# Kernel optimization log

Hardware: AMD Instinct MI355X
Metric: run time of the kernel (lower is better)

The kernel has to match this reference:

```python
import jax, jax.numpy as jnp
import numpy as np

LN_EPS = 1e-5
RMS_EPS = 1e-5

B, T, D = 4, 2048, 1024
H, DK, DV = 4, 256, 512            # head_k_dim = D/H, head_v_dim = expand_v * head_k_dim (expand_v=2)
KDIM, VDIM = H * DK, H * DV        # 1024, 2048
FFN = 4096                          # int(d_model * ffn_ratio)
CONV = 4


def _layernorm(x, w, b):
    mu = jnp.mean(x, -1, keepdims=True)
    var = jnp.mean(jnp.square(x - mu), -1, keepdims=True)
    return (x - mu) * jax.lax.rsqrt(var + LN_EPS) * w + b


def _short_conv_silu(x, w):
    # causal depthwise conv, kernel size K, then SiLU. x: [B,T,C], w: [C,K]
    K = w.shape[1]
    xp = jnp.pad(x, ((0, 0), (K - 1, 0), (0, 0)))
    y = sum(xp[:, i:i + x.shape[1], :] * w[:, i] for i in range(K))
    return jax.nn.silu(y)


def _l2norm(x):
    return x * jax.lax.rsqrt(jnp.sum(jnp.square(x), -1, keepdims=True) + 1e-6)


def _gated_delta_rule(q, k, v, g, beta):
    # q,k: [B,T,H,DK]; v: [B,T,H,DV]; g,beta: [B,T,H]
    # S_t = exp(g_t)*S_{t-1} + k_t (beta_t*(v_t - k_t^T exp(g_t) S_{t-1}))^T ; o_t = q_t^T S_t
    def step(S, inp):
        qt, kt, vt, gt, bt = inp
        S = S * jnp.exp(gt)[..., None, None]          # [B,H,DK,DV]
        mem = jnp.einsum('bhk,bhkv->bhv', kt, S)
        delta = (vt - mem) * bt[..., None]
        S = S + jnp.einsum('bhk,bhv->bhkv', kt, delta)
        o = jnp.einsum('bhk,bhkv->bhv', qt, S)
        return S, o
    S0 = jnp.zeros((q.shape[0], H, DK, DV), q.dtype)
    xs = (q.transpose(1, 0, 2, 3), k.transpose(1, 0, 2, 3), v.transpose(1, 0, 2, 3),
          g.transpose(1, 0, 2), beta.transpose(1, 0, 2))
    _, o = jax.lax.scan(step, S0, xs)
    return o.transpose(1, 0, 2, 3)  # [B,T,H,DV]


def setup_inputs() -> dict:
    key = jax.random.key(0)
    ks = jax.random.split(key, 24)
    n = lambda k, shp, s=0.02: jax.random.normal(k, shp, dtype=jnp.float32) * s
    return {
        'x': jax.random.normal(ks[0], (B, T, D), dtype=jnp.float32),
        'Wq': n(ks[1], (D, KDIM)), 'Wk': n(ks[2], (D, KDIM)), 'Wv': n(ks[3], (D, VDIM)),
        'Wa': n(ks[4], (D, H)), 'Wb': n(ks[5], (D, H)), 'Wg': n(ks[6], (D, VDIM)),
        'conv_q_w': n(ks[7], (KDIM, CONV), 0.2), 'conv_k_w': n(ks[8], (KDIM, CONV), 0.2),
        'conv_v_w': n(ks[9], (VDIM, CONV), 0.2),
        'A_log': jnp.log(jax.random.uniform(ks[10], (H,), minval=1.0, maxval=16.0, dtype=jnp.float32)),
        'dt_bias': jax.random.uniform(ks[11], (H,), minval=0.0, maxval=0.5, dtype=jnp.float32),
        'o_norm_w': jnp.ones((DV,), jnp.float32),
        'Wo': n(ks[12], (VDIM, D)),
        'ln1_w': jnp.ones((D,), jnp.float32), 'ln1_b': jnp.zeros((D,), jnp.float32),
        'ln2_w': jnp.ones((D,), jnp.float32), 'ln2_b': jnp.zeros((D,), jnp.float32),
        'ffn_w1': n(ks[13], (D, FFN)), 'ffn_b1': jnp.zeros((FFN,), jnp.float32),
        'ffn_w2': n(ks[14], (FFN, D)), 'ffn_b2': jnp.zeros((D,), jnp.float32),
    }


def reference(x, Wq, Wk, Wv, Wa, Wb, Wg, conv_q_w, conv_k_w, conv_v_w, A_log, dt_bias,
              o_norm_w, Wo, ln1_w, ln1_b, ln2_w, ln2_b, ffn_w1, ffn_b1, ffn_w2, ffn_b2):
    normed = _layernorm(x, ln1_w, ln1_b)
    q = _short_conv_silu(normed @ Wq, conv_q_w).reshape(B, T, H, DK)
    k = _short_conv_silu(normed @ Wk, conv_k_w).reshape(B, T, H, DK)
    v = _short_conv_silu(normed @ Wv, conv_v_w).reshape(B, T, H, DV)
    q = _l2norm(q) * (DK ** -0.5)
    k = _l2norm(k)
    g = -jnp.exp(A_log) * jax.nn.softplus(normed @ Wa + dt_bias)   # [B,T,H], negative
    beta = jax.nn.sigmoid(normed @ Wb)                              # [B,T,H]
    o = _gated_delta_rule(q, k, v, g, beta)                         # [B,T,H,DV]
    gate = (normed @ Wg).reshape(B, T, H, DV)
    o = o * jax.lax.rsqrt(jnp.mean(jnp.square(o), -1, keepdims=True) + RMS_EPS)
    o = o * o_norm_w * jax.nn.silu(gate)                            # gated RMSNorm
    x = x + o.reshape(B, T, VDIM) @ Wo
    h = _layernorm(x, ln2_w, ln2_b)
    ffn = jax.nn.gelu(h @ ffn_w1 + ffn_b1, approximate=False) @ ffn_w2 + ffn_b2
    return x + ffn
```

## Files before the change

### kernel.cpp

```cpp
#include <hip/hip_runtime.h>
#include <math.h>

#define B_    4
#define T_    2048
#define D_    1024
#define H_    4
#define DK_   256
#define DV_   512
#define KDIM_ 1024
#define VDIM_ 2048
#define FFN_  4096
#define BT_   8192

typedef unsigned short bf16;
typedef __attribute__((ext_vector_type(8))) short short8;
typedef __attribute__((ext_vector_type(4))) short short4v;
typedef __attribute__((ext_vector_type(4))) float f32x4;


__device__ __forceinline__ float sigmoidf_(float x) { return 1.f / (1.f + expf(-x)); }
__device__ __forceinline__ float siluf_(float x)    { return x / (1.f + expf(-x)); }
__device__ __forceinline__ float geluf_(float x)    { return 0.5f * x * (1.f + erff(x * 0.70710678118654752f)); }

__device__ __forceinline__ float bf2f(bf16 u) {
  union { unsigned int i; float f; } c; c.i = (unsigned int)u << 16; return c.f;
}
__device__ __forceinline__ bf16 f2bf(float f) {
  union { unsigned int i; float f; } c; c.f = f;
  unsigned int r = c.i + 0x7fffu + ((c.i >> 16) & 1u);
  return (bf16)(r >> 16);
}

__device__ __forceinline__ void gload16(const bf16* g, bf16* l) {
  __builtin_amdgcn_global_load_lds((__attribute__((address_space(1))) const void*)g,
                                   (__attribute__((address_space(3))) void*)l, 16, 0, 0);
}

__device__ __forceinline__ void storeC(float* p, float v) { *p = v; }
__device__ __forceinline__ void storeC(bf16* p, float v)  { *p = f2bf(v); }

__device__ __forceinline__ short8 ld76(const bf16* p) {
  union { short8 v; short4v h[2]; } u;
  u.h[0] = *(const short4v*)p;
  u.h[1] = *(const short4v*)(p + 4);
  return u.v;
}
__device__ __forceinline__ void st4bf(bf16* p, f32x4 v) {
  short4v o;
  o[0] = (short)f2bf(v[0]); o[1] = (short)f2bf(v[1]);
  o[2] = (short)f2bf(v[2]); o[3] = (short)f2bf(v[3]);
  *(short4v*)p = o;
}

__device__ __forceinline__ float block_sum256(float v, float* red) {
#pragma unroll
  for (int off = 32; off; off >>= 1) v += __shfl_xor(v, off, 64);
  __syncthreads();
  if ((threadIdx.x & 63) == 0) red[threadIdx.x >> 6] = v;
  __syncthreads();
  return red[0] + red[1] + red[2] + red[3];
}


__global__ __launch_bounds__(256) void sentinel_kernel(float* out, int n) {
  int i = blockIdx.x * 256 + threadIdx.x;
  if (i < n) out[i] = 12345.0f;
}


__global__ __launch_bounds__(256) void ln_kernel(const float* __restrict__ x,
                                                 const float* __restrict__ w,
                                                 const float* __restrict__ b,
                                                 bf16* __restrict__ y) {
  __shared__ float red[4];
  int row = blockIdx.x;
  const float* xr = x + (size_t)row * D_;
  float xv[4];
  float s = 0.f;
#pragma unroll
  for (int i = 0; i < 4; i++) { xv[i] = xr[threadIdx.x + 256 * i]; s += xv[i]; }
  float mean = block_sum256(s, red) * (1.f / D_);
  float s2 = 0.f;
#pragma unroll
  for (int i = 0; i < 4; i++) { float d = xv[i] - mean; s2 += d * d; }
  float var = block_sum256(s2, red) * (1.f / D_);
  float inv = rsqrtf(var + 1e-5f);
  bf16* yr = y + (size_t)row * D_;
#pragma unroll
  for (int i = 0; i < 4; i++) {
    int c = threadIdx.x + 256 * i;
    yr[c] = f2bf((xv[i] - mean) * inv * w[c] + b[c]);
  }
}


__global__ __launch_bounds__(256) void convT_kernel(const float* __restrict__ src,
                                                    bf16* __restrict__ dst,
                                                    int K, int N) {
  __shared__ float t[32][33];
  int n0 = blockIdx.x * 32, k0 = blockIdx.y * 32;
  int tx = threadIdx.x & 31, ty = threadIdx.x >> 5;
#pragma unroll
  for (int i = 0; i < 4; i++)
    t[ty + i * 8][tx] = src[(size_t)(k0 + ty + i * 8) * N + n0 + tx];
  __syncthreads();
#pragma unroll
  for (int i = 0; i < 4; i++)
    dst[(size_t)(n0 + ty + i * 8) * K + k0 + tx] = f2bf(t[tx][ty + i * 8]);
}


__global__ __launch_bounds__(256) void kT_kernel(const bf16* __restrict__ k16,
                                                 bf16* __restrict__ kT) {
  __shared__ bf16 tile[32][34];
  int t0 = blockIdx.x * 32;
  int d0 = blockIdx.y * 32;
  int bh = blockIdx.z;
  int b = bh >> 2, h = bh & 3;
  int tx = threadIdx.x & 31, ty = threadIdx.x >> 5;
#pragma unroll
  for (int i = 0; i < 4; i++)
    tile[ty + 8 * i][tx] = k16[(size_t)(b * T_ + t0 + ty + 8 * i) * KDIM_ + h * DK_ + d0 + tx];
  __syncthreads();
  int t = t0 + tx;
  int c = t >> 6, tb = (t >> 3) & 7, te = t & 7;
  size_t base = ((size_t)(bh * 32 + c) * 8 + tb) * 2048 + te;
#pragma unroll
  for (int i = 0; i < 4; i++)
    kT[base + (size_t)(d0 + ty + 8 * i) * 8] = tile[tx][ty + 8 * i];
}


template <typename TC>
__global__ __launch_bounds__(256) void gemm_mfma(const bf16* __restrict__ A,
                                                 const bf16* __restrict__ Bt,
                                                 const float* __restrict__ bias,
                                                 const float* __restrict__ res,
                                                 TC* __restrict__ C,
                                                 int N, int K, int flags) {
  __shared__ __align__(16) bf16 As[128 * 32];
  __shared__ __align__(16) bf16 Bs[128 * 32];
  int tid = threadIdx.x;
  int wave = tid >> 6, lane = tid & 63;
  int bm = blockIdx.y * 128, bn = blockIdx.x * 128;
  int wm = (wave >> 1) * 64, wn = (wave & 1) * 64;
  int lm = lane & 15;
  int quad = lane >> 4;

  f32x4 acc[4][4];
#pragma unroll
  for (int i = 0; i < 4; i++)
#pragma unroll
    for (int j = 0; j < 4; j++) acc[i][j] = (f32x4){0.f, 0.f, 0.f, 0.f};

  int srow = wave * 32 + (lane >> 2);
  int scol = (lane & 3) * 8;
  const bf16* ag = A  + (size_t)(bm + srow) * K + scol;
  const bf16* bg = Bt + (size_t)(bn + srow) * K + scol;
  bf16* al = As + wave * 32 * 32;
  bf16* bl = Bs + wave * 32 * 32;
  const size_t gstep = (size_t)16 * K;

  for (int k0 = 0; k0 < K; k0 += 32) {
    gload16(ag + k0,         al);
    gload16(ag + k0 + gstep, al + 16 * 32);
    gload16(bg + k0,         bl);
    gload16(bg + k0 + gstep, bl + 16 * 32);
    __syncthreads();

    short8 af[4], bf[4];
#pragma unroll
    for (int i = 0; i < 4; i++)
      af[i] = *(const short8*)&As[(wm + i * 16 + lm) * 32 + quad * 8];
#pragma unroll
    for (int j = 0; j < 4; j++)
      bf[j] = *(const short8*)&Bs[(wn + j * 16 + lm) * 32 + quad * 8];
#pragma unroll
    for (int i = 0; i < 4; i++)
#pragma unroll
      for (int j = 0; j < 4; j++)
        acc[i][j] = __builtin_amdgcn_mfma_f32_16x16x32_bf16(af[i], bf[j], acc[i][j], 0, 0, 0);
    __syncthreads();
  }

#pragma unroll
  for (int i = 0; i < 4; i++) {
    int row0 = bm + wm + i * 16 + quad * 4;
#pragma unroll
    for (int j = 0; j < 4; j++) {
      int col = bn + wn + j * 16 + lm;
      float badd = (flags & 1) ? bias[col] : 0.f;
#pragma unroll
      for (int r = 0; r < 4; r++) {
        float v = acc[i][j][r] + badd;
        if (flags & 2) v = geluf_(v);
        if (flags & 4) v += res[(size_t)(row0 + r) * N + col];
        storeC(&C[(size_t)(row0 + r) * N + col], v);
      }
    }
  }
}


__global__ __launch_bounds__(256) void ab_kernel(const bf16* __restrict__ normed,
                                                 const float* __restrict__ Wa,
                                                 const float* __restrict__ Wb,
                                                 const float* __restrict__ A_log,
                                                 const float* __restrict__ dt_bias,
                                                 float* __restrict__ g,
                                                 float* __restrict__ beta) {
  __shared__ float red[4];
  int row = blockIdx.x;
  const bf16* xr = normed + (size_t)row * D_;
  float aacc[4] = {}, bacc[4] = {};
#pragma unroll
  for (int i = 0; i < 4; i++) {
    int d = threadIdx.x + 256 * i;
    float xv = bf2f(xr[d]);
    float4 wa = *(const float4*)&Wa[d * 4];
    float4 wb = *(const float4*)&Wb[d * 4];
    aacc[0] += xv * wa.x; aacc[1] += xv * wa.y; aacc[2] += xv * wa.z; aacc[3] += xv * wa.w;
    bacc[0] += xv * wb.x; bacc[1] += xv * wb.y; bacc[2] += xv * wb.z; bacc[3] += xv * wb.w;
  }
  float sa[4], sb[4];
#pragma unroll
  for (int h = 0; h < 4; h++) {
    sa[h] = block_sum256(aacc[h], red);
    sb[h] = block_sum256(bacc[h], red);
  }
  if (threadIdx.x < 4) {
    int h = threadIdx.x;
    float xa = sa[h] + dt_bias[h];
    float sp = (xa > 20.f) ? xa : log1pf(expf(xa));
    g[row * 4 + h] = -expf(A_log[h]) * sp;
    beta[row * 4 + h] = sigmoidf_(sb[h]);
  }
}


__global__ __launch_bounds__(256) void conv_qk_kernel(const float* __restrict__ pre,
                                                      const float* __restrict__ convw,
                                                      bf16* __restrict__ out,
                                                      float scale) {
  __shared__ float red[4];
  int blk = blockIdx.x;
  int h = blk & 3;
  int bt = blk >> 2;
  int t = bt & (T_ - 1);
  int c = h * DK_ + threadIdx.x;
  float y = 0.f;
#pragma unroll
  for (int i = 0; i < 4; i++) {
    int tt = t + i - 3;
    if (tt >= 0) y += pre[(size_t)(bt + i - 3) * KDIM_ + c] * convw[c * 4 + i];
  }
  y = siluf_(y);
  float ss = block_sum256(y * y, red);
  y *= rsqrtf(ss + 1e-6f) * scale;
  out[(size_t)bt * KDIM_ + c] = f2bf(y);
}

__global__ __launch_bounds__(256) void conv_v_kernel(const float* __restrict__ pre,
                                                     const float* __restrict__ convw,
                                                     bf16* __restrict__ out) {
  int idx = blockIdx.x * 256 + threadIdx.x;
  int c = idx & (VDIM_ - 1);
  int bt = idx >> 11;
  int t = bt & (T_ - 1);
  float y = 0.f;
#pragma unroll
  for (int i = 0; i < 4; i++) {
    int tt = t + i - 3;
    if (tt >= 0) y += pre[(size_t)(bt + i - 3) * VDIM_ + c] * convw[c * 4 + i];
  }
  out[idx] = f2bf(siluf_(y));
}


#define SP 76

__global__ __launch_bounds__(256, 2) void delta_p1(const bf16* __restrict__ q,
                                                   const bf16* __restrict__ k,
                                                   const bf16* __restrict__ v,
                                                   const float* __restrict__ g,
                                                   const float* __restrict__ beta,
                                                   bf16* __restrict__ Pg,
                                                   bf16* __restrict__ Wg,
                                                   bf16* __restrict__ Yg,
                                                   float* __restrict__ gsc) {
  __shared__ bf16 Abf[64 * SP];
  __shared__ bf16 DTg[64 * SP];
  __shared__ float Ub[64 * 64];
  __shared__ float Gc[64], Lm[64], Bt[64];

  int blk = blockIdx.x;
  int c = blk & 31, bh = blk >> 5;
  int b = bh >> 2, h = bh & 3;
  int tid = threadIdx.x;
  int wave = tid >> 6, lane = tid & 63;
  int lm = lane & 15, quad = lane >> 4;
  int r0 = c * 64;

  const bf16* kb = k + (size_t)b * T_ * KDIM_ + h * DK_;
  const bf16* qb = q + (size_t)b * T_ * KDIM_ + h * DK_;
  const bf16* vb = v + (size_t)b * T_ * VDIM_ + h * DV_;
  const float* gbp = g    + (size_t)b * T_ * H_ + h;
  const float* bbp = beta + (size_t)b * T_ * H_ + h;
  size_t cb = (size_t)bh * 32 + c;
  bf16* PgC = Pg + cb * 4096;
  bf16* WgC = Wg + cb * 64 * 512;
  bf16* YgC = Yg + cb * 64 * 256;

  if (wave == 0) {
    float gv = gbp[(size_t)(r0 + lane) * H_];
    float bv = bbp[(size_t)(r0 + lane) * H_];
#pragma unroll
    for (int d = 1; d < 64; d <<= 1) {
      float nn = __shfl_up(gv, (unsigned)d, 64);
      if (lane >= d) gv += nn;
    }
    Gc[lane] = gv; Lm[lane] = expf(gv); Bt[lane] = bv;
    gsc[cb * 64 + lane] = gv;
  }
  __syncthreads();

  {
    f32x4 akk[4], aqk[4];
#pragma unroll
    for (int j = 0; j < 4; j++) { akk[j] = (f32x4){0.f,0.f,0.f,0.f}; aqk[j] = (f32x4){0.f,0.f,0.f,0.f}; }
    const bf16* krow = kb + (size_t)(r0 + 16 * wave + lm) * KDIM_;
    const bf16* qrow = qb + (size_t)(r0 + 16 * wave + lm) * KDIM_;
#pragma unroll
    for (int ks = 0; ks < 8; ks++) {
      short8 ak = *(const short8*)(krow + 8 * quad + 32 * ks);
      short8 aq = *(const short8*)(qrow + 8 * quad + 32 * ks);
#pragma unroll
      for (int j = 0; j < 4; j++) {
        short8 bk = *(const short8*)(kb + (size_t)(r0 + 16 * j + lm) * KDIM_ + 8 * quad + 32 * ks);
        akk[j] = __builtin_amdgcn_mfma_f32_16x16x32_bf16(ak, bk, akk[j], 0, 0, 0);
        aqk[j] = __builtin_amdgcn_mfma_f32_16x16x32_bf16(aq, bk, aqk[j], 0, 0, 0);
      }
    }
    float gi[4], bi[4];
#pragma unroll
    for (int r = 0; r < 4; r++) {
      int i = 16 * wave + 4 * quad + r;
      gi[r] = Gc[i]; bi[r] = Bt[i];
    }
#pragma unroll
    for (int j = 0; j < 4; j++) {
      int s = 16 * j + lm;
      float gs = Gc[s];
#pragma unroll
      for (int r = 0; r < 4; r++) {
        int i = 16 * wave + 4 * quad + r;
        float dec = expf(gi[r] - gs);
        Abf[(size_t)i * SP + s] = f2bf((s < i)  ? bi[r] * dec * akk[j][r] : 0.f);
        PgC[(size_t)i * 64 + s] = f2bf((s <= i) ? dec * aqk[j][r]        : 0.f);
      }
    }
  }

  for (int grp = 0; grp < 12; grp++) {
    __syncthreads();
    {
      int* dz = (int*)DTg;
#pragma unroll
      for (int i = 0; i < 10; i++) {
        int idx = tid + 256 * i;
        if (idx < 64 * SP / 2) dz[idx] = 0;
      }
    }
    int cg = 16 * wave + lm;
#pragma unroll
    for (int ti = 0; ti < 4; ti++)
#pragma unroll
      for (int r = 0; r < 4; r++) {
        int t = 16 * ti + 4 * quad + r;
        float val;
        if (grp < 8) val = Bt[t] * bf2f(vb[(size_t)(r0 + t) * VDIM_ + grp * 64 + cg]);
        else         val = Bt[t] * Lm[t] * bf2f(kb[(size_t)(r0 + t) * KDIM_ + (grp - 8) * 64 + cg]);
        Ub[t * 64 + cg] = val;
      }
    __syncthreads();

#pragma unroll
    for (int j = 0; j < 4; j++) {
      if (j > 0) {
        f32x4 racc = (f32x4){0.f, 0.f, 0.f, 0.f};
        int nk = (j == 3) ? 2 : 1;
        for (int ks = 0; ks < nk; ks++) {
          short8 aa = ld76(&Abf[(size_t)(16 * j + lm) * SP + 8 * quad + 32 * ks]);
          short8 bd = ld76(&DTg[(size_t)(16 * wave + lm) * SP + 8 * quad + 32 * ks]);
          racc = __builtin_amdgcn_mfma_f32_16x16x32_bf16(aa, bd, racc, 0, 0, 0);
        }
#pragma unroll
        for (int r = 0; r < 4; r++)
          Ub[(16 * j + 4 * quad + r) * 64 + 16 * wave + lm] -= racc[r];
        __syncthreads();
      }
      if (wave == 0) {
        int tl = lane & 15, sg = lane >> 4;
        short4v ab4 = *(const short4v*)&Abf[(size_t)(16 * j + tl) * SP + 16 * j + 4 * sg];
        float av[4];
        av[0] = bf2f((bf16)ab4[0]); av[1] = bf2f((bf16)ab4[1]);
        av[2] = bf2f((bf16)ab4[2]); av[3] = bf2f((bf16)ab4[3]);
        float d[16];
#pragma unroll
        for (int t = 0; t < 16; t++) {
          float val = Ub[(16 * j + t) * 64 + lane];
#pragma unroll
          for (int s = 0; s < t; s++) {
            float ats = __shfl(av[s & 3], t + 16 * (s >> 2), 64);
            val -= ats * d[s];
          }
          d[t] = val;
          DTg[(size_t)lane * SP + 16 * j + t] = f2bf(val);
        }
      }
      __syncthreads();
    }

#pragma unroll
    for (int ti = 0; ti < 4; ti++)
#pragma unroll
      for (int r = 0; r < 4; r++) {
        int t = 16 * ti + 4 * quad + r;
        bf16 val = DTg[(size_t)(16 * wave + lm) * SP + t];
        if (grp < 8) WgC[(size_t)t * 512 + grp * 64 + cg] = val;
        else         YgC[(size_t)t * 256 + (grp - 8) * 64 + cg] = val;
      }
  }
}


#define SP2 264
#define SD  72

__global__ __launch_bounds__(256, 1) void delta_p2(const bf16* __restrict__ q,
                                                   const bf16* __restrict__ kT,
                                                   const bf16* __restrict__ Wg,
                                                   const bf16* __restrict__ Yg,
                                                   const bf16* __restrict__ Pg,
                                                   const float* __restrict__ gsc,
                                                   bf16* __restrict__ o) {
  __shared__ __align__(16) bf16 ST[32 * SP2];
  __shared__ __align__(16) bf16 dT[32 * SD];
  __shared__ __align__(16) bf16 dTe[32 * SD];
  __shared__ float Gc[64];
  __shared__ __align__(16) bf16 Ks[2][8 * 256 * 8];
  __shared__ __align__(16) bf16 Ws[2][64 * 32];

  int blk = blockIdx.x;
  int bh = blk & 15, vs = blk >> 4;
  int b = bh >> 2, h = bh & 3;
  int tid = threadIdx.x;
  int wave = tid >> 6, lane = tid & 63;
  int lm = lane & 15, quad = lane >> 4;
  int rt = wave;
  int v0 = vs * 32;

  const bf16* qb  = q  + (size_t)b * T_ * KDIM_ + h * DK_;
  const bf16* kTb = kT + (size_t)bh * 32 * 16384;
  const bf16* WgB = Wg + (size_t)bh * 32 * 32768 + (size_t)(tid >> 2) * 512 + v0 + (tid & 3) * 8;
  const bf16* PgB = Pg + (size_t)bh * 32 * 4096 + (size_t)(16 * rt + lm) * 64 + 8 * quad;
  bf16*       ob  = o  + (size_t)b * T_ * VDIM_ + h * DV_ + v0;

  f32x4 Sacc[4][2];
#pragma unroll
  for (int dd = 0; dd < 4; dd++)
#pragma unroll
    for (int cc = 0; cc < 2; cc++) Sacc[dd][cc] = (f32x4){0.f, 0.f, 0.f, 0.f};

#pragma unroll
  for (int i = 0; i < 8; i++)
    gload16(kTb + i * 2048 + tid * 8, Ks[0] + i * 2048 + wave * 512);
  gload16(WgB, Ws[0] + tid * 8);
  __builtin_amdgcn_sched_barrier(0);
  short8 pfn[2];
  pfn[0] = *(const short8*)(PgB);
  pfn[1] = *(const short8*)(PgB + 32);
  __builtin_amdgcn_sched_barrier(0);
  float gnext = gsc[(size_t)bh * 2048 + lane], gnn = 0.f;
  short8 qfr[8], yfr[8];
  {
    const bf16* qrow = qb + (size_t)(16 * rt + lm) * KDIM_;
    const bf16* yrow = Yg + (size_t)bh * 32 * 16384 + (size_t)(16 * rt + lm) * 256;
#pragma unroll
    for (int kf = 0; kf < 8; kf++) {
      qfr[kf] = *(const short8*)(qrow + 8 * quad + 32 * kf);
      yfr[kf] = *(const short8*)(yrow + 8 * quad + 32 * kf);
    }
  }

  for (int c = 0; c < 32; c++) {
    const int r0 = c * 64;
    const int idx = c & 1;
    const bf16* Ksb = Ks[idx];
    const bf16* Wsb = Ws[idx];
    bf16* Ksn = Ks[idx ^ 1];
    bf16* Wsn = Ws[idx ^ 1];

#pragma unroll
    for (int dd = 0; dd < 4; dd++)
#pragma unroll
      for (int cc = 0; cc < 2; cc++)
        st4bf(&ST[(size_t)(16 * cc + lm) * SP2 + 16 * (4 * wave + dd) + 4 * quad], Sacc[dd][cc]);
    Gc[lane] = gnext;
    asm volatile("s_waitcnt lgkmcnt(0)" ::: "memory");
    __builtin_amdgcn_s_barrier();

    f32x4 Yacc[2], Oacc[2];
#pragma unroll
    for (int cc = 0; cc < 2; cc++) { Yacc[cc] = (f32x4){0.f,0.f,0.f,0.f}; Oacc[cc] = (f32x4){0.f,0.f,0.f,0.f}; }
#pragma unroll
    for (int cc = 0; cc < 2; cc++) {
      short8 Bs[8];
#pragma unroll
      for (int kf = 0; kf < 8; kf++)
        Bs[kf] = *(const short8*)&ST[(size_t)(16 * cc + lm) * SP2 + 8 * quad + 32 * kf];
#pragma unroll
      for (int kf = 0; kf < 8; kf++) {
        Yacc[cc] = __builtin_amdgcn_mfma_f32_16x16x32_bf16(yfr[kf], Bs[kf], Yacc[cc], 0, 0, 0);
        Oacc[cc] = __builtin_amdgcn_mfma_f32_16x16x32_bf16(qfr[kf], Bs[kf], Oacc[cc], 0, 0, 0);
      }
    }
    __builtin_amdgcn_sched_barrier(0);

    {
      int cn = (c + 1) & 31;
      size_t cbn = (size_t)bh * 32 + cn;
      const bf16* slab = kTb + (size_t)cn * 16384;
#pragma unroll
      for (int i = 0; i < 8; i++)
        gload16(slab + i * 2048 + tid * 8, Ksn + i * 2048 + wave * 512);
      gload16(WgB + (size_t)cn * 32768, Wsn + tid * 8);
      __builtin_amdgcn_sched_barrier(0);
      gnn = gsc[cbn * 64 + lane];
      const bf16* qrow = qb + (size_t)(cn * 64 + 16 * rt + lm) * KDIM_;
      const bf16* yrow = Yg + cbn * 16384 + (size_t)(16 * rt + lm) * 256;
#pragma unroll
      for (int kf = 0; kf < 8; kf++) {
        qfr[kf] = *(const short8*)(qrow + 8 * quad + 32 * kf);
        yfr[kf] = *(const short8*)(yrow + 8 * quad + 32 * kf);
      }
    }
    __builtin_amdgcn_sched_barrier(0);

    asm volatile("" : : "v"(*(const int*)&pfn[0]), "v"(*(const int*)&pfn[1]) : "memory");
    __builtin_amdgcn_sched_barrier(0);
    float g63 = Gc[63];
    float lamv[4], erv[4];
#pragma unroll
    for (int rr = 0; rr < 4; rr++) {
      float gr = Gc[16 * rt + 4 * quad + rr];
      lamv[rr] = __expf(gr);
      erv[rr]  = __expf(g63 - gr);
    }
#pragma unroll
    for (int cc = 0; cc < 2; cc++) {
      short4v dpack, depack;
#pragma unroll
      for (int rr = 0; rr < 4; rr++) {
        int row = 16 * rt + 4 * quad + rr;
        float dv = bf2f(Wsb[row * 32 + 16 * cc + lm]) - Yacc[cc][rr];
        Oacc[cc][rr] *= lamv[rr];
        dpack[rr]  = (short)f2bf(dv);
        depack[rr] = (short)f2bf(dv * erv[rr]);
      }
      *(short4v*)&dT [(size_t)(16 * cc + lm) * SD + 16 * rt + 4 * quad] = dpack;
      *(short4v*)&dTe[(size_t)(16 * cc + lm) * SD + 16 * rt + 4 * quad] = depack;
    }
    asm volatile("s_waitcnt lgkmcnt(0)" ::: "memory");
    __builtin_amdgcn_s_barrier();

    float lend = __expf(g63);
    short8 Be[2][2];
#pragma unroll
    for (int cc = 0; cc < 2; cc++)
#pragma unroll
      for (int kf = 0; kf < 2; kf++)
        Be[cc][kf] = ld76(&dTe[(size_t)(16 * cc + lm) * SD + 8 * quad + 32 * kf]);
#pragma unroll
    for (int dd = 0; dd < 4; dd++) {
      int Dt = 4 * wave + dd;
#pragma unroll
      for (int cc = 0; cc < 2; cc++) {
        f32x4 s = Sacc[dd][cc];
        s[0] *= lend; s[1] *= lend; s[2] *= lend; s[3] *= lend;
#pragma unroll
        for (int kf = 0; kf < 2; kf++) {
          short8 ka = *(const short8*)&Ksb[((size_t)(quad + 4 * kf) * 256 + 16 * Dt + lm) * 8];
          s = __builtin_amdgcn_mfma_f32_16x16x32_bf16(ka, Be[cc][kf], s, 0, 0, 0);
        }
        Sacc[dd][cc] = s;
      }
    }

#pragma unroll
    for (int cc = 0; cc < 2; cc++) {
#pragma unroll
      for (int kf = 0; kf < 2; kf++) {
        short8 bd = ld76(&dT[(size_t)(16 * cc + lm) * SD + 8 * quad + 32 * kf]);
        Oacc[cc] = __builtin_amdgcn_mfma_f32_16x16x32_bf16(pfn[kf], bd, Oacc[cc], 0, 0, 0);
      }
#pragma unroll
      for (int rr = 0; rr < 4; rr++) {
        int row = 16 * rt + 4 * quad + rr;
        ob[(size_t)(r0 + row) * VDIM_ + 16 * cc + lm] = f2bf(Oacc[cc][rr]);
      }
    }
    __builtin_amdgcn_sched_barrier(0);

    {
      int cn = (c + 1) & 31;
      const bf16* pc = PgB + (size_t)cn * 4096;
      pfn[0] = *(const short8*)(pc);
      pfn[1] = *(const short8*)(pc + 32);
    }
    gnext = gnn;
    asm volatile("s_waitcnt lgkmcnt(0)" ::: "memory");
    __builtin_amdgcn_s_barrier();
  }
}


__global__ __launch_bounds__(256) void gated_rms_kernel(bf16* __restrict__ o,
                                                        const bf16* __restrict__ gate,
                                                        const float* __restrict__ onw) {
  __shared__ float red[4];
  int blk = blockIdx.x;
  int h = blk & 3;
  int bt = blk >> 2;
  size_t base = (size_t)bt * VDIM_ + h * DV_;
  int tid = threadIdx.x;
  float o1 = bf2f(o[base + tid]), o2 = bf2f(o[base + tid + 256]);
  float ss = block_sum256(o1 * o1 + o2 * o2, red);
  float s = rsqrtf(ss * (1.f / DV_) + 1e-5f);
  float g1 = bf2f(gate[base + tid]), g2 = bf2f(gate[base + tid + 256]);
  o[base + tid]       = f2bf(o1 * s * onw[tid] * siluf_(g1));
  o[base + tid + 256] = f2bf(o2 * s * onw[tid + 256] * siluf_(g2));
}


extern "C" void kernel_launch(void* const* d_in, const int* in_sizes, int n_in,
                              void* d_out, int out_size, void* d_ws, size_t ws_size,
                              hipStream_t stream) {
  const float* x        = (const float*)d_in[0];
  const float* Wq       = (const float*)d_in[1];
  const float* Wk       = (const float*)d_in[2];
  const float* Wv       = (const float*)d_in[3];
  const float* Wa       = (const float*)d_in[4];
  const float* Wb       = (const float*)d_in[5];
  const float* Wg       = (const float*)d_in[6];
  const float* conv_q_w = (const float*)d_in[7];
  const float* conv_k_w = (const float*)d_in[8];
  const float* conv_v_w = (const float*)d_in[9];
  const float* A_log    = (const float*)d_in[10];
  const float* dt_bias  = (const float*)d_in[11];
  const float* o_norm_w = (const float*)d_in[12];
  const float* Wo       = (const float*)d_in[13];
  const float* ln1_w    = (const float*)d_in[14];
  const float* ln1_b    = (const float*)d_in[15];
  const float* ln2_w    = (const float*)d_in[16];
  const float* ln2_b    = (const float*)d_in[17];
  const float* ffn_w1   = (const float*)d_in[18];
  const float* ffn_b1   = (const float*)d_in[19];
  const float* ffn_w2   = (const float*)d_in[20];
  const float* ffn_b2   = (const float*)d_in[21];

  size_t required = (size_t)218 << 20;
  if (ws_size < required) {
    sentinel_kernel<<<(out_size + 255) / 256, 256, 0, stream>>>((float*)d_out, out_size);
    return;
  }

  char* base = (char*)d_ws;
  float* pre    = (float*)(base);
  bf16*  normed = (bf16*)(base + ((size_t)64  << 20));
  bf16*  q16    = (bf16*)(base + ((size_t)80  << 20));
  bf16*  k16    = (bf16*)(base + ((size_t)96  << 20));
  bf16*  v16    = (bf16*)(base + ((size_t)112 << 20));
  bf16*  g16    = (bf16*)(base + ((size_t)144 << 20));
  bf16*  o16    = (bf16*)(base + ((size_t)176 << 20));
  bf16*  wslot  = (bf16*)(base + ((size_t)208 << 20));
  float* gvec   = (float*)(base + ((size_t)216 << 20));
  float* bvec   = gvec + (size_t)BT_ * H_;
  float* gsc    = (float*)(base + ((size_t)217 << 20));
  bf16*  Yg     = (bf16*)(base);
  bf16*  Wgb    = (bf16*)(base + ((size_t)16 << 20));
  bf16*  Pg     = (bf16*)(base + ((size_t)48 << 20));
  bf16*  kTg    = (bf16*)(base + ((size_t)52 << 20));
  float* x2     = (float*)(base);
  bf16*  hb16   = (bf16*)(base + ((size_t)64  << 20));
  bf16*  ffn1   = (bf16*)(base + ((size_t)80  << 20));

  ln_kernel<<<BT_, 256, 0, stream>>>(x, ln1_w, ln1_b, normed);

  convT_kernel<<<dim3(KDIM_ / 32, D_ / 32), 256, 0, stream>>>(Wq, wslot, D_, KDIM_);
  gemm_mfma<float><<<dim3(KDIM_ / 128, BT_ / 128), 256, 0, stream>>>(normed, wslot, nullptr, nullptr, pre, KDIM_, D_, 0);
  conv_qk_kernel<<<BT_ * H_, 256, 0, stream>>>(pre, conv_q_w, q16, 0.0625f);

  convT_kernel<<<dim3(KDIM_ / 32, D_ / 32), 256, 0, stream>>>(Wk, wslot, D_, KDIM_);
  gemm_mfma<float><<<dim3(KDIM_ / 128, BT_ / 128), 256, 0, stream>>>(normed, wslot, nullptr, nullptr, pre, KDIM_, D_, 0);
  conv_qk_kernel<<<BT_ * H_, 256, 0, stream>>>(pre, conv_k_w, k16, 1.0f);

  convT_kernel<<<dim3(VDIM_ / 32, D_ / 32), 256, 0, stream>>>(Wv, wslot, D_, VDIM_);
  gemm_mfma<float><<<dim3(VDIM_ / 128, BT_ / 128), 256, 0, stream>>>(normed, wslot, nullptr, nullptr, pre, VDIM_, D_, 0);
  conv_v_kernel<<<(BT_ * VDIM_) / 256, 256, 0, stream>>>(pre, conv_v_w, v16);

  convT_kernel<<<dim3(VDIM_ / 32, D_ / 32), 256, 0, stream>>>(Wg, wslot, D_, VDIM_);
  gemm_mfma<bf16><<<dim3(VDIM_ / 128, BT_ / 128), 256, 0, stream>>>(normed, wslot, nullptr, nullptr, g16, VDIM_, D_, 0);

  ab_kernel<<<BT_, 256, 0, stream>>>(normed, Wa, Wb, A_log, dt_bias, gvec, bvec);

  kT_kernel<<<dim3(T_ / 32, DK_ / 32, 16), 256, 0, stream>>>(k16, kTg);
  delta_p1<<<512, 256, 0, stream>>>(q16, k16, v16, gvec, bvec, Pg, Wgb, Yg, gsc);
  delta_p2<<<256, 256, 0, stream>>>(q16, kTg, Wgb, Yg, Pg, gsc, o16);

  gated_rms_kernel<<<BT_ * H_, 256, 0, stream>>>(o16, g16, o_norm_w);

  convT_kernel<<<dim3(D_ / 32, VDIM_ / 32), 256, 0, stream>>>(Wo, wslot, VDIM_, D_);
  gemm_mfma<float><<<dim3(D_ / 128, BT_ / 128), 256, 0, stream>>>(o16, wslot, nullptr, x, x2, D_, VDIM_, 4);

  ln_kernel<<<BT_, 256, 0, stream>>>(x2, ln2_w, ln2_b, hb16);

  convT_kernel<<<dim3(FFN_ / 32, D_ / 32), 256, 0, stream>>>(ffn_w1, wslot, D_, FFN_);
  gemm_mfma<bf16><<<dim3(FFN_ / 128, BT_ / 128), 256, 0, stream>>>(hb16, wslot, ffn_b1, nullptr, ffn1, FFN_, D_, 1 | 2);
  convT_kernel<<<dim3(D_ / 32, FFN_ / 32), 256, 0, stream>>>(ffn_w2, wslot, FFN_, D_);
  gemm_mfma<float><<<dim3(D_ / 128, BT_ / 128), 256, 0, stream>>>(ffn1, wslot, ffn_b2, x2, (float*)d_out, D_, FFN_, 1 | 4);
}
```

Measured before the change: 1.178 ms.

## Precompute chunk triangular inverse once and apply via MFMA per column group

Instead of running the serial forward-substitution triangular solve for each of the 12 column groups of V and K in delta_p1, the kernel now solves once against an identity to build the inverse matrix M = (I+A)^-1 in LDS. Each group then becomes a bf16 MFMA product of M with the beta-scaled U tile. This removes the long single-wave serial solves and their many barriers per group. In exchange the inverse is rounded to bf16 and applied as a separate GEMM, which may change numerics slightly, and barriers use raw s_barrier with explicit waitcnt.

```diff
diff --git a/kernel.cpp b/kernel.cpp
--- a/kernel.cpp
+++ b/kernel.cpp
@@ -277,7 +277,9 @@
 }
 
 
-#define SP 76
+#define SP  76
+#define UBP 72
+#define MTP 68
 
 __global__ __launch_bounds__(256, 2) void delta_p1(const bf16* __restrict__ q,
                                                    const bf16* __restrict__ k,
@@ -290,7 +292,9 @@
                                                    float* __restrict__ gsc) {
   __shared__ bf16 Abf[64 * SP];
   __shared__ bf16 DTg[64 * SP];
-  __shared__ float Ub[64 * 64];
+  __shared__ __align__(8) bf16 MT[64 * MTP];
+  __shared__ __align__(8) bf16 Ubt[64 * UBP];
+  __shared__ float UbJ[16 * 64];
   __shared__ float Gc[64], Lm[64], Bt[64];
 
   int blk = blockIdx.x;
@@ -322,6 +326,14 @@
     Gc[lane] = gv; Lm[lane] = expf(gv); Bt[lane] = bv;
     gsc[cb * 64 + lane] = gv;
   }
+  {
+    int* dz = (int*)DTg;
+#pragma unroll
+    for (int i = 0; i < 10; i++) {
+      int idx = tid + 256 * i;
+      if (idx < 64 * SP / 2) dz[idx] = 0;
+    }
+  }
   __syncthreads();
 
   {
@@ -360,76 +372,97 @@
       }
     }
   }
-
+  __syncthreads();
+
+#pragma unroll 1
+  for (int j = 0; j < 4; j++) {
+#pragma unroll
+    for (int i = 0; i < 4; i++) {
+      int idx = tid + 256 * i;
+      int row = idx >> 6, col = idx & 63;
+      UbJ[row * 64 + col] = (col == 16 * j + row) ? 1.f : 0.f;
+    }
+    __syncthreads();
+    if (j > 0) {
+      f32x4 racc = (f32x4){0.f, 0.f, 0.f, 0.f};
+      int nk = (j == 3) ? 2 : 1;
+      for (int ks = 0; ks < nk; ks++) {
+        short8 aa = ld76(&Abf[(size_t)(16 * j + lm) * SP + 8 * quad + 32 * ks]);
+        short8 bd = ld76(&DTg[(size_t)(16 * wave + lm) * SP + 8 * quad + 32 * ks]);
+        racc = __builtin_amdgcn_mfma_f32_16x16x32_bf16(aa, bd, racc, 0, 0, 0);
+      }
+#pragma unroll
+      for (int r = 0; r < 4; r++)
+        UbJ[(4 * quad + r) * 64 + 16 * wave + lm] -= racc[r];
+      __syncthreads();
+    }
+    if (wave == 0) {
+      int tl = lane & 15, sg = lane >> 4;
+      short4v ab4 = *(const short4v*)&Abf[(size_t)(16 * j + tl) * SP + 16 * j + 4 * sg];
+      float av[4];
+      av[0] = bf2f((bf16)ab4[0]); av[1] = bf2f((bf16)ab4[1]);
+      av[2] = bf2f((bf16)ab4[2]); av[3] = bf2f((bf16)ab4[3]);
+      float d[16];
+#pragma unroll
+      for (int t = 0; t < 16; t++) {
+        float val = UbJ[t * 64 + lane];
+#pragma unroll
+        for (int s = 0; s < t; s++) {
+          float ats = __shfl(av[s & 3], t + 16 * (s >> 2), 64);
+          val -= ats * d[s];
+        }
+        d[t] = val;
+        bf16 vb16 = f2bf(val);
+        DTg[(size_t)lane * SP + 16 * j + t] = vb16;
+        MT [(size_t)(16 * j + t) * MTP + lane] = vb16;
+      }
+    }
+    __syncthreads();
+  }
+
+  int cg = 16 * wave + lm;
+#pragma unroll 1
   for (int grp = 0; grp < 12; grp++) {
-    __syncthreads();
-    {
-      int* dz = (int*)DTg;
-#pragma unroll
-      for (int i = 0; i < 10; i++) {
-        int idx = tid + 256 * i;
-        if (idx < 64 * SP / 2) dz[idx] = 0;
-      }
-    }
-    int cg = 16 * wave + lm;
-#pragma unroll
-    for (int ti = 0; ti < 4; ti++)
+#pragma unroll
+    for (int ti = 0; ti < 4; ti++) {
+      short4v up;
 #pragma unroll
       for (int r = 0; r < 4; r++) {
         int t = 16 * ti + 4 * quad + r;
         float val;
         if (grp < 8) val = Bt[t] * bf2f(vb[(size_t)(r0 + t) * VDIM_ + grp * 64 + cg]);
         else         val = Bt[t] * Lm[t] * bf2f(kb[(size_t)(r0 + t) * KDIM_ + (grp - 8) * 64 + cg]);
-        Ub[t * 64 + cg] = val;
-      }
-    __syncthreads();
-
-#pragma unroll
-    for (int j = 0; j < 4; j++) {
-      if (j > 0) {
-        f32x4 racc = (f32x4){0.f, 0.f, 0.f, 0.f};
-        int nk = (j == 3) ? 2 : 1;
-        for (int ks = 0; ks < nk; ks++) {
-          short8 aa = ld76(&Abf[(size_t)(16 * j + lm) * SP + 8 * quad + 32 * ks]);
-          short8 bd = ld76(&DTg[(size_t)(16 * wave + lm) * SP + 8 * quad + 32 * ks]);
-          racc = __builtin_amdgcn_mfma_f32_16x16x32_bf16(aa, bd, racc, 0, 0, 0);
-        }
-#pragma unroll
-        for (int r = 0; r < 4; r++)
-          Ub[(16 * j + 4 * quad + r) * 64 + 16 * wave + lm] -= racc[r];
-        __syncthreads();
-      }
-      if (wave == 0) {
-        int tl = lane & 15, sg = lane >> 4;
-        short4v ab4 = *(const short4v*)&Abf[(size_t)(16 * j + tl) * SP + 16 * j + 4 * sg];
-        float av[4];
-        av[0] = bf2f((bf16)ab4[0]); av[1] = bf2f((bf16)ab4[1]);
-        av[2] = bf2f((bf16)ab4[2]); av[3] = bf2f((bf16)ab4[3]);
-        float d[16];
-#pragma unroll
-        for (int t = 0; t < 16; t++) {
-          float val = Ub[(16 * j + t) * 64 + lane];
-#pragma unroll
-          for (int s = 0; s < t; s++) {
-            float ats = __shfl(av[s & 3], t + 16 * (s >> 2), 64);
-            val -= ats * d[s];
-          }
-          d[t] = val;
-          DTg[(size_t)lane * SP + 16 * j + t] = f2bf(val);
-        }
-      }
-      __syncthreads();
-    }
-
-#pragma unroll
-    for (int ti = 0; ti < 4; ti++)
-#pragma unroll
-      for (int r = 0; r < 4; r++) {
-        int t = 16 * ti + 4 * quad + r;
-        bf16 val = DTg[(size_t)(16 * wave + lm) * SP + t];
-        if (grp < 8) WgC[(size_t)t * 512 + grp * 64 + cg] = val;
-        else         YgC[(size_t)t * 256 + (grp - 8) * 64 + cg] = val;
-      }
+        up[r] = (short)f2bf(val);
+      }
+      *(short4v*)&Ubt[(size_t)cg * UBP + 16 * ti + 4 * quad] = up;
+    }
+    asm volatile("s_waitcnt lgkmcnt(0)" ::: "memory");
+    __builtin_amdgcn_s_barrier();
+
+    f32x4 racc[4];
+#pragma unroll
+    for (int jt = 0; jt < 4; jt++) racc[jt] = (f32x4){0.f, 0.f, 0.f, 0.f};
+#pragma unroll
+    for (int ks = 0; ks < 2; ks++) {
+      short8 aM = ld76(&MT[(size_t)(16 * wave + lm) * MTP + 8 * quad + 32 * ks]);
+#pragma unroll
+      for (int jt = 0; jt < 4; jt++) {
+        short8 bU = ld76(&Ubt[(size_t)(16 * jt + lm) * UBP + 8 * quad + 32 * ks]);
+        racc[jt] = __builtin_amdgcn_mfma_f32_16x16x32_bf16(aM, bU, racc[jt], 0, 0, 0);
+      }
+    }
+#pragma unroll
+    for (int jt = 0; jt < 4; jt++) {
+#pragma unroll
+      for (int rr = 0; rr < 4; rr++) {
+        int t = 16 * wave + 4 * quad + rr;
+        int cc = 16 * jt + lm;
+        if (grp < 8) WgC[(size_t)t * 512 + grp * 64 + cc]       = f2bf(racc[jt][rr]);
+        else         YgC[(size_t)t * 256 + (grp - 8) * 64 + cc] = f2bf(racc[jt][rr]);
+      }
+    }
+    asm volatile("s_waitcnt lgkmcnt(0)" ::: "memory");
+    __builtin_amdgcn_s_barrier();
   }
 }
 
```

Result: faster. 1.101 ms (-6.6%).
